# Kernel tuning notes

Hardware: AMD Instinct MI355X
Metric: run time of the kernel (lower is better)

Reference implementation:

```python
import jax
import jax.numpy as jnp
from jax import lax
import numpy as np

DIM = 64
EPS = 1e-5
DN = ('NCDHW', 'OIDHW', 'NCDHW')


def setup_inputs() -> dict:
    key = jax.random.key(0)
    ks = jax.random.split(key, 4)
    x = jax.random.normal(ks[0], (2, DIM, 64, 64, 64), dtype=jnp.float32)
    gamma = jnp.ones((DIM,), jnp.float32)
    beta = jnp.zeros((DIM,), jnp.float32)
    w0 = jax.random.normal(ks[1], (DIM, 1, 5, 5, 5), jnp.float32) * 0.1
    b0 = jnp.zeros((DIM,), jnp.float32)
    ws = jax.random.normal(ks[2], (DIM, 1, 7, 7, 7), jnp.float32) * 0.05
    bs = jnp.zeros((DIM,), jnp.float32)
    w1 = jax.random.normal(ks[3], (DIM, DIM, 1, 1, 1), jnp.float32) * 0.1
    b1 = jnp.zeros((DIM,), jnp.float32)
    return {"x": x, "gamma": gamma, "beta": beta, "w0": w0, "b0": b0,
            "ws": ws, "bs": bs, "w1": w1, "b1": b1}


def _cb(b):
    # broadcast per-channel vector over NCDHW
    return b.reshape(1, -1, 1, 1, 1)


def reference(x, gamma, beta, w0, b0, ws, bs, w1, b1):
    dim = x.shape[1]
    # BatchNorm (training mode, biased variance) over N, D, H, W per channel
    mean = jnp.mean(x, axis=(0, 2, 3, 4), keepdims=True)
    var = jnp.var(x, axis=(0, 2, 3, 4), keepdims=True)
    xn = (x - mean) * lax.rsqrt(var + EPS) * _cb(gamma) + _cb(beta)
    # depthwise conv3d k=5, pad=2 (same)
    attn = lax.conv_general_dilated(xn, w0, (1, 1, 1), [(2, 2)] * 3,
                                    feature_group_count=dim,
                                    dimension_numbers=DN) + _cb(b0)
    # dilated depthwise conv3d k=7, dilation=3, pad=9 (same)
    attn = lax.conv_general_dilated(attn, ws, (1, 1, 1), [(9, 9)] * 3,
                                    rhs_dilation=(3, 3, 3),
                                    feature_group_count=dim,
                                    dimension_numbers=DN) + _cb(bs)
    # pointwise 1x1x1 conv
    attn = lax.conv_general_dilated(attn, w1, (1, 1, 1), [(0, 0)] * 3,
                                    dimension_numbers=DN) + _cb(b1)
    # gated multiply with residual input (u = x.clone())
    return x * attn
```

## Files before the change

kernel.cpp:

```cpp
#include <hip/hip_runtime.h>
#include <math.h>

#define C_DIM 64
#define N_B 2
#define SPATIAL (64*64*64)
#define PLANE_SZ (64*64)
#define EPSV 1e-5f

__global__ __launch_bounds__(256) void k_stats(const float* __restrict__ x,
                                               float* __restrict__ wsf) {
    int c = blockIdx.x >> 4;
    int part = blockIdx.x & 15;
    int tid = threadIdx.x;
    const int per_part = SPATIAL / 16;
    float s = 0.f, sq = 0.f;
    for (int n = 0; n < N_B; ++n) {
        const float* base = x + ((size_t)(n * C_DIM + c)) * SPATIAL + (size_t)part * per_part;
        const float4* b4 = (const float4*)base;
        #pragma unroll
        for (int it = 0; it < 16; ++it) {
            float4 v = b4[it * 256 + tid];
            s  += v.x + v.y + v.z + v.w;
            sq += v.x*v.x + v.y*v.y + v.z*v.z + v.w*v.w;
        }
    }
    __shared__ float rs[256], rq[256];
    rs[tid] = s; rq[tid] = sq;
    __syncthreads();
    for (int off = 128; off > 0; off >>= 1) {
        if (tid < off) { rs[tid] += rs[tid+off]; rq[tid] += rq[tid+off]; }
        __syncthreads();
    }
    if (tid == 0) {
        atomicAdd(&wsf[c], rs[0]);
        atomicAdd(&wsf[64 + c], rq[0]);
    }
}

__global__ void k_finalize(float* __restrict__ wsf,
                           const float* __restrict__ gamma,
                           const float* __restrict__ beta) {
    int c = threadIdx.x;
    float cnt = (float)(N_B * SPATIAL);
    float mean = wsf[c] / cnt;
    float var = wsf[64 + c] / cnt - mean * mean;
    float sc = gamma[c] * rsqrtf(var + EPSV);
    wsf[128 + c] = sc;
    wsf[192 + c] = beta[c] - mean * sc;
}

#define K2D 12
#define K2H 12
#define K2W 36
__global__ __launch_bounds__(256) void k_conv5(const float* __restrict__ x,
                                               const float* __restrict__ w0,
                                               const float* __restrict__ b0,
                                               const float* __restrict__ wsf,
                                               float* __restrict__ attn0) {
    __shared__ float sh[K2D * K2H * K2W];
    __shared__ float wt[125];
    int tid = threadIdx.x;
    int tx = tid & 31;
    int ty = tid >> 5;
    int wtile = blockIdx.x;
    int dt = blockIdx.y & 7;
    int ht = blockIdx.y >> 3;
    int nc = blockIdx.z;
    int c = nc & 63;
    int w0i = wtile * 32;
    int h0 = ht * 8;
    int d0 = dt * 8;
    const float* xb = x + (size_t)nc * SPATIAL;
    float sc = wsf[128 + c], shv = wsf[192 + c];
    if (tid < 125) wt[tid] = w0[c * 125 + tid];
    for (int idx = tid; idx < K2D * K2H * K2W; idx += 256) {
        int z = idx / (K2H * K2W);
        int rem = idx - z * (K2H * K2W);
        int y = rem / K2W;
        int xw = rem - y * K2W;
        int gd = d0 - 2 + z, gh = h0 - 2 + y, gw = w0i - 2 + xw;
        float v = 0.f;
        if ((unsigned)gd < 64u && (unsigned)gh < 64u && (unsigned)gw < 64u)
            v = xb[(size_t)gd * PLANE_SZ + gh * 64 + gw] * sc + shv;
        sh[idx] = v;
    }
    __syncthreads();
    float acc[8] = {0,0,0,0,0,0,0,0};
    #pragma unroll
    for (int z = 0; z < 12; ++z) {
        #pragma unroll
        for (int j = 0; j < 5; ++j) {
            #pragma unroll
            for (int k = 0; k < 5; ++k) {
                float v = sh[(z * K2H + (ty + j)) * K2W + tx + k];
                #pragma unroll
                for (int i = 0; i < 5; ++i) {
                    int dz = z - i;
                    if (dz >= 0 && dz < 8)
                        acc[dz] += wt[(i * 5 + j) * 5 + k] * v;
                }
            }
        }
    }
    float bias = b0[c];
    float* ob = attn0 + (size_t)nc * SPATIAL + (size_t)(h0 + ty) * 64 + w0i + tx;
    #pragma unroll
    for (int dz = 0; dz < 8; ++dz)
        ob[(size_t)(d0 + dz) * PLANE_SZ] = acc[dz] + bias;
}

#define ROWS7 26
#define COLS7 84
#define S7_ELEMS (ROWS7 * COLS7)
#define S7_ITERS 5
#define S7_BUF 2560

template<int P>
__device__ __forceinline__ void conv7_stage(const float* __restrict__ ab,
                                            const float* __restrict__ wc,
                                            float* __restrict__ sh,
                                            int tid, int hh, int w,
                                            int j0, int rd,
                                            const int (&goff)[S7_ITERS],
                                            const float (&gmsk)[S7_ITERS],
                                            float (&acc)[8]) {
    float* cur = sh + (P & 1) * S7_BUF;
    float* nxt = sh + ((P + 1) & 1) * S7_BUF;
    int mP = j0 - 3 + P;
    int zP = 3 * mP + rd;
    bool zokP = (mP >= 0) && (zP < 64);
    int mN = mP + 1;
    int zN = zP + 3;
    bool zokN = (P < 13) && (mN >= 0) && (zN < 64);

    float r[S7_ITERS];
    if (zokN) {
        const float* pb = ab + (size_t)zN * PLANE_SZ;
        #pragma unroll
        for (int k = 0; k < S7_ITERS; ++k)
            r[k] = pb[goff[k]];
    }
    if (zokP) {
        #pragma unroll
        for (int v = 0; v < 7; ++v) {
            float val[7];
            int rb = (hh + 3 * v) * COLS7 + w;
            #pragma unroll
            for (int u = 0; u < 7; ++u) val[u] = cur[rb + 3 * u];
            #pragma unroll
            for (int t = 0; t < 7; ++t) {
                const int q = P - t;
                if (q >= 0 && q < 8) {
                    #pragma unroll
                    for (int u = 0; u < 7; ++u)
                        acc[q] = fmaf(wc[t * 49 + v * 7 + u], val[u], acc[q]);
                }
            }
        }
    }
    if (zokN) {
        #pragma unroll
        for (int k = 0; k < S7_ITERS; ++k)
            nxt[k * 512 + tid] = r[k] * gmsk[k];
    }
    __syncthreads();
}

__global__ __launch_bounds__(512, 4) void k_conv7(const float* __restrict__ attn0,
                                                  const float* __restrict__ wsv,
                                                  const float* __restrict__ bs,
                                                  float* __restrict__ attn1) {
    __shared__ float sh[2 * S7_BUF];
    int tid = threadIdx.x;
    int w = tid & 63;
    int hh = tid >> 6;
    int ht = blockIdx.x;
    int rd = blockIdx.y % 3;
    int j0 = (blockIdx.y / 3) * 8;
    int nc = blockIdx.z;
    int c = nc & 63;
    int h0 = ht * 8;
    int h = h0 + hh;
    const float* ab = attn0 + (size_t)nc * SPATIAL;
    const float* wc = wsv + c * 343;

    int goff[S7_ITERS];
    float gmsk[S7_ITERS];
    #pragma unroll
    for (int k = 0; k < S7_ITERS; ++k) {
        int idx = k * 512 + tid;
        int row = idx / COLS7;
        int col = idx - row * COLS7;
        int gy = h0 - 9 + row;
        int gx = col - 9;
        bool valid = (idx < S7_ELEMS) && (col < 82) &&
                     ((unsigned)gy < 64u) && ((unsigned)gx < 64u);
        goff[k] = valid ? (gy * 64 + gx) : 0;
        gmsk[k] = valid ? 1.f : 0.f;
    }

    {
        int m0 = j0 - 3;
        int z0 = 3 * m0 + rd;
        if (m0 >= 0 && z0 < 64) {
            const float* pb = ab + (size_t)z0 * PLANE_SZ;
            #pragma unroll
            for (int k = 0; k < S7_ITERS; ++k)
                sh[k * 512 + tid] = pb[goff[k]] * gmsk[k];
        }
        __syncthreads();
    }

    float acc[8] = {0,0,0,0,0,0,0,0};

    conv7_stage< 0>(ab, wc, sh, tid, hh, w, j0, rd, goff, gmsk, acc);
    conv7_stage< 1>(ab, wc, sh, tid, hh, w, j0, rd, goff, gmsk, acc);
    conv7_stage< 2>(ab, wc, sh, tid, hh, w, j0, rd, goff, gmsk, acc);
    conv7_stage< 3>(ab, wc, sh, tid, hh, w, j0, rd, goff, gmsk, acc);
    conv7_stage< 4>(ab, wc, sh, tid, hh, w, j0, rd, goff, gmsk, acc);
    conv7_stage< 5>(ab, wc, sh, tid, hh, w, j0, rd, goff, gmsk, acc);
    conv7_stage< 6>(ab, wc, sh, tid, hh, w, j0, rd, goff, gmsk, acc);
    conv7_stage< 7>(ab, wc, sh, tid, hh, w, j0, rd, goff, gmsk, acc);
    conv7_stage< 8>(ab, wc, sh, tid, hh, w, j0, rd, goff, gmsk, acc);
    conv7_stage< 9>(ab, wc, sh, tid, hh, w, j0, rd, goff, gmsk, acc);
    conv7_stage<10>(ab, wc, sh, tid, hh, w, j0, rd, goff, gmsk, acc);
    conv7_stage<11>(ab, wc, sh, tid, hh, w, j0, rd, goff, gmsk, acc);
    conv7_stage<12>(ab, wc, sh, tid, hh, w, j0, rd, goff, gmsk, acc);
    conv7_stage<13>(ab, wc, sh, tid, hh, w, j0, rd, goff, gmsk, acc);

    float bias = bs[c];
    float* ob = attn1 + (size_t)nc * SPATIAL + (size_t)h * 64 + w;
    #pragma unroll
    for (int q = 0; q < 8; ++q) {
        int d = 3 * (j0 + q) + rd;
        if (d < 64)
            ob[(size_t)d * PLANE_SZ] = acc[q] + bias;
    }
}

__global__ __launch_bounds__(256) void k_pointwise(const float* __restrict__ attn1,
                                                   const float* __restrict__ x,
                                                   const float* __restrict__ w1,
                                                   const float* __restrict__ b1,
                                                   float* __restrict__ out) {
    __shared__ float at[64 * 64];
    int tid = threadIdx.x;
    int sl = tid & 63;
    int cg = __builtin_amdgcn_readfirstlane(tid >> 6);
    int s0 = blockIdx.x * 64;
    int n = blockIdx.y;
    const float* a_base = attn1 + (size_t)n * C_DIM * SPATIAL + s0;
    #pragma unroll
    for (int it = 0; it < 16; ++it) {
        int idx = it * 256 + tid;
        int row = idx >> 6;
        at[idx] = a_base[(size_t)row * SPATIAL + sl];
    }
    __syncthreads();
    float acc[16];
    #pragma unroll
    for (int j = 0; j < 16; ++j) acc[j] = 0.f;
    for (int ci = 0; ci < 64; ++ci) {
        float va = at[ci * 64 + sl];
        #pragma unroll
        for (int j = 0; j < 16; ++j) {
            int cc = cg * 16 + j;
            acc[j] += w1[cc * 64 + ci] * va;
        }
    }
    const float* xb = x + (size_t)n * C_DIM * SPATIAL + s0;
    float* ob = out + (size_t)n * C_DIM * SPATIAL + s0;
    #pragma unroll
    for (int j = 0; j < 16; ++j) {
        int cc = cg * 16 + j;
        float attn = acc[j] + b1[cc];
        ob[(size_t)cc * SPATIAL + sl] = xb[(size_t)cc * SPATIAL + sl] * attn;
    }
}

extern "C" void kernel_launch(void* const* d_in, const int* in_sizes, int n_in,
                              void* d_out, int out_size, void* d_ws, size_t ws_size,
                              hipStream_t stream) {
    const float* x     = (const float*)d_in[0];
    const float* gamma = (const float*)d_in[1];
    const float* beta  = (const float*)d_in[2];
    const float* w0    = (const float*)d_in[3];
    const float* b0    = (const float*)d_in[4];
    const float* wsv   = (const float*)d_in[5];
    const float* bs    = (const float*)d_in[6];
    const float* w1    = (const float*)d_in[7];
    const float* b1    = (const float*)d_in[8];
    float* out = (float*)d_out;
    float* wsf = (float*)d_ws;
    float* attn1 = wsf + 256;

    hipMemsetAsync(d_ws, 0, 1024, stream);
    k_stats<<<dim3(1024), dim3(256), 0, stream>>>(x, wsf);
    k_finalize<<<dim3(1), dim3(64), 0, stream>>>(wsf, gamma, beta);
    k_conv5<<<dim3(2, 64, 128), dim3(256), 0, stream>>>(x, w0, b0, wsf, out);
    k_conv7<<<dim3(8, 9, 128), dim3(512), 0, stream>>>(out, wsv, bs, attn1);
    k_pointwise<<<dim3(4096, 2), dim3(256), 0, stream>>>(attn1, x, w1, b1, out);
}
```

Measured before the change: 1.152 ms.

## Stream full depth per residue class in dilated conv7 to remove halo reloads

The dilated 7x7x7 depthwise conv kernel now has each block walk the entire depth of one residue class (22 output planes) instead of 8 output planes with a 6-plane halo. Each input plane is loaded into shared memory once and scattered into 22 accumulators. The grid shrinks from 9 to 3 blocks along y. This removes redundant halo plane loads and barrier stages, but raises register pressure (22 accumulators under launch bounds 512,4) and cuts block-level parallelism by three.

```diff
diff --git a/kernel.cpp b/kernel.cpp
--- a/kernel.cpp
+++ b/kernel.cpp
@@ -114,28 +114,25 @@
 #define S7_ELEMS (ROWS7 * COLS7)
 #define S7_ITERS 5
 #define S7_BUF 2560
+#define NJ7 22
 
 template<int P>
 __device__ __forceinline__ void conv7_stage(const float* __restrict__ ab,
                                             const float* __restrict__ wc,
                                             float* __restrict__ sh,
-                                            int tid, int hh, int w,
-                                            int j0, int rd,
+                                            int tid, int hh, int w, int rd,
                                             const int (&goff)[S7_ITERS],
                                             const float (&gmsk)[S7_ITERS],
-                                            float (&acc)[8]) {
+                                            float (&acc)[NJ7]) {
     float* cur = sh + (P & 1) * S7_BUF;
     float* nxt = sh + ((P + 1) & 1) * S7_BUF;
-    int mP = j0 - 3 + P;
-    int zP = 3 * mP + rd;
-    bool zokP = (mP >= 0) && (zP < 64);
-    int mN = mP + 1;
-    int zN = zP + 3;
-    bool zokN = (P < 13) && (mN >= 0) && (zN < 64);
+    int zP = 3 * P + rd;
+    bool zokP = (zP < 64);
+    bool zokN = (P < 21) && (zP + 3 < 64);
 
     float r[S7_ITERS];
     if (zokN) {
-        const float* pb = ab + (size_t)zN * PLANE_SZ;
+        const float* pb = ab + (size_t)(zP + 3) * PLANE_SZ;
         #pragma unroll
         for (int k = 0; k < S7_ITERS; ++k)
             r[k] = pb[goff[k]];
@@ -148,12 +145,13 @@
             #pragma unroll
             for (int u = 0; u < 7; ++u) val[u] = cur[rb + 3 * u];
             #pragma unroll
-            for (int t = 0; t < 7; ++t) {
-                const int q = P - t;
-                if (q >= 0 && q < 8) {
+            for (int s = 0; s < 7; ++s) {
+                const int j = P - 3 + s;
+                if (j >= 0 && j < NJ7) {
                     #pragma unroll
                     for (int u = 0; u < 7; ++u)
-                        acc[q] = fmaf(wc[t * 49 + v * 7 + u], val[u], acc[q]);
+                        acc[j] = fmaf(wc[(6 - s) * 49 + v * 7 + u],
+                                      val[u], acc[j]);
                 }
             }
         }
@@ -175,8 +173,7 @@
     int w = tid & 63;
     int hh = tid >> 6;
     int ht = blockIdx.x;
-    int rd = blockIdx.y % 3;
-    int j0 = (blockIdx.y / 3) * 8;
+    int rd = blockIdx.y;
     int nc = blockIdx.z;
     int c = nc & 63;
     int h0 = ht * 8;
@@ -200,41 +197,47 @@
     }
 
     {
-        int m0 = j0 - 3;
-        int z0 = 3 * m0 + rd;
-        if (m0 >= 0 && z0 < 64) {
-            const float* pb = ab + (size_t)z0 * PLANE_SZ;
-            #pragma unroll
-            for (int k = 0; k < S7_ITERS; ++k)
-                sh[k * 512 + tid] = pb[goff[k]] * gmsk[k];
-        }
-        __syncthreads();
-    }
-
-    float acc[8] = {0,0,0,0,0,0,0,0};
-
-    conv7_stage< 0>(ab, wc, sh, tid, hh, w, j0, rd, goff, gmsk, acc);
-    conv7_stage< 1>(ab, wc, sh, tid, hh, w, j0, rd, goff, gmsk, acc);
-    conv7_stage< 2>(ab, wc, sh, tid, hh, w, j0, rd, goff, gmsk, acc);
-    conv7_stage< 3>(ab, wc, sh, tid, hh, w, j0, rd, goff, gmsk, acc);
-    conv7_stage< 4>(ab, wc, sh, tid, hh, w, j0, rd, goff, gmsk, acc);
-    conv7_stage< 5>(ab, wc, sh, tid, hh, w, j0, rd, goff, gmsk, acc);
-    conv7_stage< 6>(ab, wc, sh, tid, hh, w, j0, rd, goff, gmsk, acc);
-    conv7_stage< 7>(ab, wc, sh, tid, hh, w, j0, rd, goff, gmsk, acc);
-    conv7_stage< 8>(ab, wc, sh, tid, hh, w, j0, rd, goff, gmsk, acc);
-    conv7_stage< 9>(ab, wc, sh, tid, hh, w, j0, rd, goff, gmsk, acc);
-    conv7_stage<10>(ab, wc, sh, tid, hh, w, j0, rd, goff, gmsk, acc);
-    conv7_stage<11>(ab, wc, sh, tid, hh, w, j0, rd, goff, gmsk, acc);
-    conv7_stage<12>(ab, wc, sh, tid, hh, w, j0, rd, goff, gmsk, acc);
-    conv7_stage<13>(ab, wc, sh, tid, hh, w, j0, rd, goff, gmsk, acc);
+        const float* pb = ab + (size_t)rd * PLANE_SZ;
+        #pragma unroll
+        for (int k = 0; k < S7_ITERS; ++k)
+            sh[k * 512 + tid] = pb[goff[k]] * gmsk[k];
+    }
+    __syncthreads();
+
+    float acc[NJ7];
+    #pragma unroll
+    for (int j = 0; j < NJ7; ++j) acc[j] = 0.f;
+
+    conv7_stage< 0>(ab, wc, sh, tid, hh, w, rd, goff, gmsk, acc);
+    conv7_stage< 1>(ab, wc, sh, tid, hh, w, rd, goff, gmsk, acc);
+    conv7_stage< 2>(ab, wc, sh, tid, hh, w, rd, goff, gmsk, acc);
+    conv7_stage< 3>(ab, wc, sh, tid, hh, w, rd, goff, gmsk, acc);
+    conv7_stage< 4>(ab, wc, sh, tid, hh, w, rd, goff, gmsk, acc);
+    conv7_stage< 5>(ab, wc, sh, tid, hh, w, rd, goff, gmsk, acc);
+    conv7_stage< 6>(ab, wc, sh, tid, hh, w, rd, goff, gmsk, acc);
+    conv7_stage< 7>(ab, wc, sh, tid, hh, w, rd, goff, gmsk, acc);
+    conv7_stage< 8>(ab, wc, sh, tid, hh, w, rd, goff, gmsk, acc);
+    conv7_stage< 9>(ab, wc, sh, tid, hh, w, rd, goff, gmsk, acc);
+    conv7_stage<10>(ab, wc, sh, tid, hh, w, rd, goff, gmsk, acc);
+    conv7_stage<11>(ab, wc, sh, tid, hh, w, rd, goff, gmsk, acc);
+    conv7_stage<12>(ab, wc, sh, tid, hh, w, rd, goff, gmsk, acc);
+    conv7_stage<13>(ab, wc, sh, tid, hh, w, rd, goff, gmsk, acc);
+    conv7_stage<14>(ab, wc, sh, tid, hh, w, rd, goff, gmsk, acc);
+    conv7_stage<15>(ab, wc, sh, tid, hh, w, rd, goff, gmsk, acc);
+    conv7_stage<16>(ab, wc, sh, tid, hh, w, rd, goff, gmsk, acc);
+    conv7_stage<17>(ab, wc, sh, tid, hh, w, rd, goff, gmsk, acc);
+    conv7_stage<18>(ab, wc, sh, tid, hh, w, rd, goff, gmsk, acc);
+    conv7_stage<19>(ab, wc, sh, tid, hh, w, rd, goff, gmsk, acc);
+    conv7_stage<20>(ab, wc, sh, tid, hh, w, rd, goff, gmsk, acc);
+    conv7_stage<21>(ab, wc, sh, tid, hh, w, rd, goff, gmsk, acc);
 
     float bias = bs[c];
     float* ob = attn1 + (size_t)nc * SPATIAL + (size_t)h * 64 + w;
     #pragma unroll
-    for (int q = 0; q < 8; ++q) {
-        int d = 3 * (j0 + q) + rd;
+    for (int j = 0; j < NJ7; ++j) {
+        int d = 3 * j + rd;
         if (d < 64)
-            ob[(size_t)d * PLANE_SZ] = acc[q] + bias;
+            ob[(size_t)d * PLANE_SZ] = acc[j] + bias;
     }
 }
 
@@ -298,6 +301,6 @@
     k_stats<<<dim3(1024), dim3(256), 0, stream>>>(x, wsf);
     k_finalize<<<dim3(1), dim3(64), 0, stream>>>(wsf, gamma, beta);
     k_conv5<<<dim3(2, 64, 128), dim3(256), 0, stream>>>(x, w0, b0, wsf, out);
-    k_conv7<<<dim3(8, 9, 128), dim3(512), 0, stream>>>(out, wsv, bs, attn1);
+    k_conv7<<<dim3(8, 3, 128), dim3(512), 0, stream>>>(out, wsv, bs, attn1);
     k_pointwise<<<dim3(4096, 2), dim3(256), 0, stream>>>(attn1, x, w1, b1, out);
 }
```

Result: slower. 1.820 ms (+58.0%).
